# Optimization experiments

Hardware: AMD Instinct MI355X
Metric: run time of the kernel (lower is better)

Reference implementation:

```python
import jax, jax.numpy as jnp
import numpy as np

ERR = 1e-12


def setup_inputs() -> dict:
    key = jax.random.key(0)
    k1, k2, k3 = jax.random.split(key, 3)
    B, H, L, D = 2, 16, 2048, 64
    k = jax.random.normal(k1, (B, H, L, D), dtype=jnp.float32)
    src = jax.random.uniform(k2, (B, H, L), dtype=jnp.float32)
    dest = jax.random.uniform(k3, (B, H, L), dtype=jnp.float32)
    return {"k": k, "src": src, "dest": dest}


def reference(k, src, dest):
    # k: [B,H,L,D], src/dest: [B,H,L]
    L = k.shape[-2]
    s = jnp.sqrt(src + ERR)   # sqrt-scaled source weights
    d = jnp.sqrt(dest + ERR)  # sqrt-scaled destination weights
    # affinity_1[b,h,i,j] = s_i * d_j * (k_i . k_j), fused as (k*s) @ (k*d)^T
    a1 = jnp.einsum("bhid,bhjd->bhij", k * s[..., :, None], k * d[..., :, None])
    # relu then (x+err)^(2/3)  (kernel: exp2(log2(relu(a)+err) * 2/3))
    a3 = jnp.exp2(jnp.log2(jax.nn.relu(a1) + ERR) * (2.0 / 3.0))
    # forward cumulative sum over j, output causally masked to j >= i
    cs = jnp.cumsum(a3, axis=-1)
    idx = jnp.arange(L)
    mask = idx[:, None] <= idx[None, :]  # keep j >= i
    return jnp.where(mask, cs, 0.0)
```

## Files before the change

### kernel.cpp

```cpp
#include <hip/hip_runtime.h>

#define BH   32
#define LSEQ 2048
#define DDIM 64
#define ERRC 1e-12f
#define SROW2 260

typedef __attribute__((ext_vector_type(8)))  short bf16x8;
typedef __attribute__((ext_vector_type(4)))  float floatx4;
typedef __attribute__((ext_vector_type(4)))  unsigned short ushort4v;

__device__ __forceinline__ unsigned short f2bf(float f) {
    unsigned u = __float_as_uint(f);
    u = u + 0x7FFFu + ((u >> 16) & 1u);
    return (unsigned short)(u >> 16);
}

__device__ __forceinline__ bf16x8 pack8s(const float* __restrict__ p, float w) {
    const floatx4* pv = (const floatx4*)p;
    floatx4 x = pv[0], y = pv[1];
    bf16x8 r;
    r[0] = (short)f2bf(x[0] * w); r[1] = (short)f2bf(x[1] * w);
    r[2] = (short)f2bf(x[2] * w); r[3] = (short)f2bf(x[3] * w);
    r[4] = (short)f2bf(y[0] * w); r[5] = (short)f2bf(y[1] * w);
    r[6] = (short)f2bf(y[2] * w); r[7] = (short)f2bf(y[3] * w);
    return r;
}

__global__ __launch_bounds__(256) void prep_kd(const float* __restrict__ k,
                                               const float* __restrict__ dest,
                                               unsigned short* __restrict__ kd) {
    int idx4 = blockIdx.x * 256 + threadIdx.x;
    int row  = idx4 >> 4;
    float d = sqrtf(dest[row] + ERRC);
    floatx4 v = ((const floatx4*)k)[idx4];
    ushort4v od;
#pragma unroll
    for (int r = 0; r < 4; ++r) od[r] = f2bf(v[r] * d);
    ((ushort4v*)kd)[idx4] = od;
}

__device__ __forceinline__ void load_frag(const unsigned short* __restrict__ p,
                                          bf16x8& lo, bf16x8& hi) {
    lo = *(const bf16x8*)p;
    hi = *(const bf16x8*)(p + 32);
}

__device__ __forceinline__ void load_b_raw(const float* __restrict__ k,
                                           const float* __restrict__ src,
                                           int bhL, int row, int q,
                                           bf16x8& lo, bf16x8& hi) {
    const float* p = k + (long)(bhL + row) * DDIM + q * 8;
    float s = sqrtf(src[bhL + row] + ERRC);
    lo = pack8s(p, s);
    hi = pack8s(p + 32, s);
}

__global__ __launch_bounds__(256, 4) void strip_sums(const unsigned short* __restrict__ kd,
                                                     const float* __restrict__ k,
                                                     const float* __restrict__ src,
                                                     float* __restrict__ S) {
    const int tid  = threadIdx.x;
    const int wave = tid >> 6;
    const int lane = tid & 63;
    const int q    = lane >> 4;
    const int l16  = lane & 15;
    const int bh   = blockIdx.x & 31;
    const int ib   = blockIdx.x >> 5;
    const int i0   = (ib * 4 + wave) * 16;
    const int bhL  = bh * LSEQ;
    const unsigned short* kdb = kd + (long)bh * LSEQ * DDIM;

    bf16x8 blo, bhi;
    load_b_raw(k, src, bhL, i0 + l16, q, blo, bhi);

    bf16x8 aLo[4], aHi[4];
#pragma unroll
    for (int t = 0; t < 4; ++t)
        load_frag(kdb + (long)(16 * t + l16) * DDIM + q * 8, aLo[t], aHi[t]);

    const float c23 = 2.0f / 3.0f;
    float ssv[3];

    for (int cc = 0; cc < 3; ++cc) {
        float ss = 0.f;
        for (int g = 0; g < 8; ++g) {
            const int jn = (cc * 8 + g < 23) ? (cc * 512 + g * 64 + 64) : 0;
            bf16x8 nLo[4], nHi[4];
#pragma unroll
            for (int t = 0; t < 4; ++t)
                load_frag(kdb + (long)(jn + 16 * t + l16) * DDIM + q * 8, nLo[t], nHi[t]);

            floatx4 acc[4];
#pragma unroll
            for (int t = 0; t < 4; ++t) {
                floatx4 z4 = {0.f, 0.f, 0.f, 0.f};
                z4 = __builtin_amdgcn_mfma_f32_16x16x32_bf16(aLo[t], blo, z4, 0, 0, 0);
                acc[t] = __builtin_amdgcn_mfma_f32_16x16x32_bf16(aHi[t], bhi, z4, 0, 0, 0);
            }

            float s = 0.f;
#pragma unroll
            for (int t = 0; t < 4; ++t)
#pragma unroll
                for (int r = 0; r < 4; ++r) {
                    float v = fmaxf(acc[t][r], 0.f) + ERRC;
                    s += exp2f(c23 * __log2f(v));
                }
            float s1 = s + __shfl_xor(s, 16, 64);
            ss += s1 + __shfl_xor(s1, 32, 64);

#pragma unroll
            for (int t = 0; t < 4; ++t) { aLo[t] = nLo[t]; aHi[t] = nHi[t]; }
        }
        ssv[cc] = ss;
    }

    float sv = (q == 0) ? ssv[0] : (q == 1) ? ssv[1] : ssv[2];
    if (q < 3)
        S[(long)(bhL + i0 + l16) * 4 + q] = sv;
}

__global__ __launch_bounds__(128, 2) void chunk_out(const unsigned short* __restrict__ kd,
                                                    const float* __restrict__ k,
                                                    const float* __restrict__ src,
                                                    const float* __restrict__ S,
                                                    float* __restrict__ out) {
    __shared__ float strip[2][16 * SROW2];
    const int tid  = threadIdx.x;
    const int wave = tid >> 6;
    const int lane = tid & 63;
    const int q    = lane >> 4;
    const int l16  = lane & 15;
    const int bh   = blockIdx.x & 31;
    const int rr   = blockIdx.x >> 5;
    const int ib2  = rr & 63;
    const int c    = rr >> 6;
    const int i0   = (ib2 * 2 + wave) * 16;
    const int bhL  = bh * LSEQ;
    const int jb   = c << 9;

    if (jb + 512 <= i0) {
        const floatx4 z = {0.f, 0.f, 0.f, 0.f};
#pragma unroll
        for (int s = 0; s < 16; ++s) {
            float* row = out + (long)(bhL + i0 + s) * LSEQ + jb + 4 * lane;
            *(floatx4*)row = z;
            *(floatx4*)(row + 256) = z;
        }
        return;
    }

    const unsigned short* kdb = kd + (long)bh * LSEQ * DDIM;
    float* sw = strip[wave];

    bf16x8 blo, bhi;
    load_b_raw(k, src, bhL, i0 + l16, q, blo, bhi);

    float carry = 0.f;
    const float* Sr = S + (long)(bhL + i0 + l16) * 4;
#pragma unroll
    for (int cc = 0; cc < 3; ++cc)
        if (cc < c) carry += Sr[cc];

    const float c23 = 2.0f / 3.0f;

    bf16x8 aLo[4], aHi[4];
#pragma unroll
    for (int t = 0; t < 4; ++t)
        load_frag(kdb + (long)(jb + 16 * t + l16) * DDIM + q * 8, aLo[t], aHi[t]);

    for (int hh = 0; hh < 2; ++hh) {
#pragma unroll
        for (int gg = 0; gg < 4; ++gg) {
            const int colbase = gg * 64;
            const int j0 = jb + hh * 256 + colbase;
            const int jl = hh * 256 + colbase + 64;
            const int jn = jb + ((jl < 512) ? jl : 0);

            bf16x8 nLo[4], nHi[4];
#pragma unroll
            for (int t = 0; t < 4; ++t)
                load_frag(kdb + (long)(jn + 16 * t + l16) * DDIM + q * 8, nLo[t], nHi[t]);

            floatx4 acc[4];
#pragma unroll
            for (int t = 0; t < 4; ++t) {
                floatx4 z4 = {0.f, 0.f, 0.f, 0.f};
                z4 = __builtin_amdgcn_mfma_f32_16x16x32_bf16(aLo[t], blo, z4, 0, 0, 0);
                acc[t] = __builtin_amdgcn_mfma_f32_16x16x32_bf16(aHi[t], bhi, z4, 0, 0, 0);
            }

            float u[4][4];
#pragma unroll
            for (int t = 0; t < 4; ++t)
#pragma unroll
                for (int r = 0; r < 4; ++r) {
                    float v = fmaxf(acc[t][r], 0.f) + ERRC;
                    u[t][r] = exp2f(c23 * __log2f(v));
                }

            if (j0 + 64 <= i0) {
                float s = 0.f;
#pragma unroll
                for (int t = 0; t < 4; ++t)
                    s += (u[t][0] + u[t][1]) + (u[t][2] + u[t][3]);
                float s1 = s + __shfl_xor(s, 16, 64);
                carry += s1 + __shfl_xor(s1, 32, 64);
                const floatx4 z = {0.f, 0.f, 0.f, 0.f};
#pragma unroll
                for (int t = 0; t < 4; ++t)
                    *(floatx4*)&sw[l16 * SROW2 + colbase + 16 * t + 4 * q] = z;
            } else {
#pragma unroll
                for (int t = 0; t < 4; ++t) {
                    const int jt0 = j0 + 16 * t;
                    float* dst = &sw[l16 * SROW2 + colbase + 16 * t + 4 * q];
                    if (jt0 + 16 <= i0) {
                        float s = (u[t][0] + u[t][1]) + (u[t][2] + u[t][3]);
                        float s1 = s + __shfl_xor(s, 16, 64);
                        carry += s1 + __shfl_xor(s1, 32, 64);
                        const floatx4 z = {0.f, 0.f, 0.f, 0.f};
                        *(floatx4*)dst = z;
                    } else {
                        u[t][1] += u[t][0];
                        u[t][2] += u[t][1];
                        u[t][3] += u[t][2];
                        const float Sg  = u[t][3];
                        const float x16 = __shfl_xor(Sg, 16, 64);
                        const float s1  = Sg + x16;
                        const float x32 = __shfl_xor(s1, 32, 64);
                        const float E = ((q & 1) ? x16 : 0.f) + ((q & 2) ? x32 : 0.f) + carry;
                        carry += s1 + x32;
                        floatx4 o;
                        if (jt0 == i0) {
#pragma unroll
                            for (int r = 0; r < 4; ++r)
                                o[r] = ((q * 4 + r) >= l16) ? (u[t][r] + E) : 0.f;
                        } else {
#pragma unroll
                            for (int r = 0; r < 4; ++r)
                                o[r] = u[t][r] + E;
                        }
                        *(floatx4*)dst = o;
                    }
                }
            }

#pragma unroll
            for (int t = 0; t < 4; ++t) { aLo[t] = nLo[t]; aHi[t] = nHi[t]; }
        }

#pragma unroll
        for (int s = 0; s < 16; ++s) {
            floatx4 v = *(const floatx4*)&sw[s * SROW2 + 4 * lane];
            *(floatx4*)(out + (long)(bhL + i0 + s) * LSEQ + jb + hh * 256 + 4 * lane) = v;
        }
    }
}

__device__ __forceinline__ void load_row16_raw(const float* __restrict__ kp, long base, int row,
                                               int q, const float* __restrict__ w, int bhL,
                                               bf16x8& lo, bf16x8& hi) {
    const float* p = kp + base + (long)row * DDIM + q * 8;
    float s = sqrtf(w[bhL + row] + ERRC);
    lo = pack8s(p, s);
    hi = pack8s(p + 32, s);
}

__global__ __launch_bounds__(256, 4) void mha_raw(const float* __restrict__ kp,
                                                  const float* __restrict__ src,
                                                  const float* __restrict__ dest,
                                                  float* __restrict__ out) {
    const int tid  = threadIdx.x;
    const int wave = tid >> 6;
    const int lane = tid & 63;
    const int q    = lane >> 4;
    const int l16  = lane & 15;
    const int bh = blockIdx.x & 31;
    const int ib = blockIdx.x >> 5;
    const int i0 = (ib * 4 + wave) * 16;
    const int bhL = bh * LSEQ;
    const long base = (long)bh * LSEQ * DDIM;

    bf16x8 blo, bhi;
    load_row16_raw(kp, base, i0 + l16, q, src, bhL, blo, bhi);

    float carry = 0.f;
    const float c23 = 2.0f / 3.0f;

    bf16x8 aLo[4], aHi[4];
#pragma unroll
    for (int t = 0; t < 4; ++t)
        load_row16_raw(kp, base, 16 * t + l16, q, dest, bhL, aLo[t], aHi[t]);

    float* orow = out + (long)(bhL + i0 + l16) * LSEQ + q * 4;

    for (int it = 0; it < 32; ++it) {
        const int j0 = it << 6;
        bf16x8 nLo[4], nHi[4];
        const int jn = (it < 31) ? (j0 + 64) : 0;
#pragma unroll
        for (int t = 0; t < 4; ++t)
            load_row16_raw(kp, base, jn + 16 * t + l16, q, dest, bhL, nLo[t], nHi[t]);

        floatx4 acc[4];
#pragma unroll
        for (int t = 0; t < 4; ++t) {
            floatx4 z4 = {0.f, 0.f, 0.f, 0.f};
            z4 = __builtin_amdgcn_mfma_f32_16x16x32_bf16(aLo[t], blo, z4, 0, 0, 0);
            acc[t] = __builtin_amdgcn_mfma_f32_16x16x32_bf16(aHi[t], bhi, z4, 0, 0, 0);
        }

        float u[4][4];
#pragma unroll
        for (int t = 0; t < 4; ++t)
#pragma unroll
            for (int r = 0; r < 4; ++r) {
                float v = fmaxf(acc[t][r], 0.f) + ERRC;
                u[t][r] = exp2f(c23 * __log2f(v));
            }

#pragma unroll
        for (int t = 0; t < 4; ++t) {
            const int jt0 = j0 + 16 * t;
            if (jt0 + 16 <= i0) {
                float s = (u[t][0] + u[t][1]) + (u[t][2] + u[t][3]);
                float s1 = s + __shfl_xor(s, 16, 64);
                carry += s1 + __shfl_xor(s1, 32, 64);
                const floatx4 z = {0.f, 0.f, 0.f, 0.f};
                *(floatx4*)(orow + jt0) = z;
            } else {
                u[t][1] += u[t][0];
                u[t][2] += u[t][1];
                u[t][3] += u[t][2];
                const float Sg  = u[t][3];
                const float x16 = __shfl_xor(Sg, 16, 64);
                const float s1  = Sg + x16;
                const float x32 = __shfl_xor(s1, 32, 64);
                const float E = ((q & 1) ? x16 : 0.f) + ((q & 2) ? x32 : 0.f) + carry;
                carry += s1 + x32;
                floatx4 o;
                if (jt0 == i0) {
#pragma unroll
                    for (int r = 0; r < 4; ++r)
                        o[r] = ((q * 4 + r) >= l16) ? (u[t][r] + E) : 0.f;
                } else {
#pragma unroll
                    for (int r = 0; r < 4; ++r)
                        o[r] = u[t][r] + E;
                }
                *(floatx4*)(orow + jt0) = o;
            }
        }

#pragma unroll
        for (int t = 0; t < 4; ++t) { aLo[t] = nLo[t]; aHi[t] = nHi[t]; }
    }
}

extern "C" void kernel_launch(void* const* d_in, const int* in_sizes, int n_in,
                              void* d_out, int out_size, void* d_ws, size_t ws_size,
                              hipStream_t stream) {
    const float* k    = (const float*)d_in[0];
    const float* src  = (const float*)d_in[1];
    const float* dest = (const float*)d_in[2];
    float* out = (float*)d_out;

    const size_t kdsz = (size_t)BH * LSEQ * DDIM * sizeof(unsigned short);
    const size_t ssz  = (size_t)BH * LSEQ * 4 * sizeof(float);
    if (ws_size >= kdsz + ssz) {
        unsigned short* kd = (unsigned short*)d_ws;
        float* S = (float*)((char*)d_ws + kdsz);
        prep_kd<<<dim3(4096), dim3(256), 0, stream>>>(k, dest, kd);
        strip_sums<<<dim3(1024), dim3(256), 0, stream>>>(kd, k, src, S);
        chunk_out<<<dim3(8192), dim3(128), 0, stream>>>(kd, k, src, S, out);
    } else {
        mha_raw<<<dim3(1024), dim3(256), 0, stream>>>(k, src, dest, out);
    }
}
```

Measured before the change: 685.7 us.

## Write chunk outputs directly from registers, drop LDS staging, remap block indices

The output kernel no longer stages each 16x256 strip in shared memory and copies it out row-coalesced. Each lane now writes its 16-byte fragments straight to global memory. Removing the LDS lets launch bounds rise to four blocks per SM. Block-to-work mapping is also reordered so adjacent waves cover the four column chunks of the same rows and head, which changes locality and the order work is scheduled. The risk is that the direct writes are less coalesced (each lane writes a different row), which may hurt write efficiency on a write-bound kernel.

```diff
diff --git a/kernel.cpp b/kernel.cpp
--- a/kernel.cpp
+++ b/kernel.cpp
@@ -4,7 +4,6 @@
 #define LSEQ 2048
 #define DDIM 64
 #define ERRC 1e-12f
-#define SROW2 260
 
 typedef __attribute__((ext_vector_type(8)))  short bf16x8;
 typedef __attribute__((ext_vector_type(4)))  float floatx4;
@@ -121,22 +120,21 @@
         S[(long)(bhL + i0 + l16) * 4 + q] = sv;
 }
 
-__global__ __launch_bounds__(128, 2) void chunk_out(const unsigned short* __restrict__ kd,
-                                                    const float* __restrict__ k,
-                                                    const float* __restrict__ src,
-                                                    const float* __restrict__ S,
-                                                    float* __restrict__ out) {
-    __shared__ float strip[2][16 * SROW2];
+__global__ __launch_bounds__(128, 4) void chunk_out2(const unsigned short* __restrict__ kd,
+                                                     const float* __restrict__ k,
+                                                     const float* __restrict__ src,
+                                                     const float* __restrict__ S,
+                                                     float* __restrict__ out) {
     const int tid  = threadIdx.x;
     const int wave = tid >> 6;
     const int lane = tid & 63;
     const int q    = lane >> 4;
     const int l16  = lane & 15;
-    const int bh   = blockIdx.x & 31;
-    const int rr   = blockIdx.x >> 5;
-    const int ib2  = rr & 63;
-    const int c    = rr >> 6;
-    const int i0   = (ib2 * 2 + wave) * 16;
+    const int u    = blockIdx.x * 2 + wave;
+    const int c    = u & 3;
+    const int bh   = (u >> 2) & 31;
+    const int it   = u >> 7;
+    const int i0   = it << 4;
     const int bhL  = bh * LSEQ;
     const int jb   = c << 9;
 
@@ -152,7 +150,6 @@
     }
 
     const unsigned short* kdb = kd + (long)bh * LSEQ * DDIM;
-    float* sw = strip[wave];
 
     bf16x8 blo, bhi;
     load_b_raw(k, src, bhL, i0 + l16, q, blo, bhi);
@@ -170,92 +167,82 @@
     for (int t = 0; t < 4; ++t)
         load_frag(kdb + (long)(jb + 16 * t + l16) * DDIM + q * 8, aLo[t], aHi[t]);
 
-    for (int hh = 0; hh < 2; ++hh) {
-#pragma unroll
-        for (int gg = 0; gg < 4; ++gg) {
-            const int colbase = gg * 64;
-            const int j0 = jb + hh * 256 + colbase;
-            const int jl = hh * 256 + colbase + 64;
-            const int jn = jb + ((jl < 512) ? jl : 0);
-
-            bf16x8 nLo[4], nHi[4];
+    float* orow = out + (long)(bhL + i0 + l16) * LSEQ + q * 4;
+
+    for (int g = 0; g < 8; ++g) {
+        const int j0 = jb + (g << 6);
+        const int jn = jb + ((g < 7) ? ((g + 1) << 6) : 0);
+
+        bf16x8 nLo[4], nHi[4];
+#pragma unroll
+        for (int t = 0; t < 4; ++t)
+            load_frag(kdb + (long)(jn + 16 * t + l16) * DDIM + q * 8, nLo[t], nHi[t]);
+
+        floatx4 acc[4];
+#pragma unroll
+        for (int t = 0; t < 4; ++t) {
+            floatx4 z4 = {0.f, 0.f, 0.f, 0.f};
+            z4 = __builtin_amdgcn_mfma_f32_16x16x32_bf16(aLo[t], blo, z4, 0, 0, 0);
+            acc[t] = __builtin_amdgcn_mfma_f32_16x16x32_bf16(aHi[t], bhi, z4, 0, 0, 0);
+        }
+
+        float uu[4][4];
+#pragma unroll
+        for (int t = 0; t < 4; ++t)
+#pragma unroll
+            for (int r = 0; r < 4; ++r) {
+                float v = fmaxf(acc[t][r], 0.f) + ERRC;
+                uu[t][r] = exp2f(c23 * __log2f(v));
+            }
+
+        if (j0 + 64 <= i0) {
+            float s = 0.f;
 #pragma unroll
             for (int t = 0; t < 4; ++t)
-                load_frag(kdb + (long)(jn + 16 * t + l16) * DDIM + q * 8, nLo[t], nHi[t]);
-
-            floatx4 acc[4];
+                s += (uu[t][0] + uu[t][1]) + (uu[t][2] + uu[t][3]);
+            float s1 = s + __shfl_xor(s, 16, 64);
+            carry += s1 + __shfl_xor(s1, 32, 64);
+            const floatx4 z = {0.f, 0.f, 0.f, 0.f};
+#pragma unroll
+            for (int t = 0; t < 4; ++t)
+                *(floatx4*)(orow + j0 + 16 * t) = z;
+        } else {
 #pragma unroll
             for (int t = 0; t < 4; ++t) {
-                floatx4 z4 = {0.f, 0.f, 0.f, 0.f};
-                z4 = __builtin_amdgcn_mfma_f32_16x16x32_bf16(aLo[t], blo, z4, 0, 0, 0);
-                acc[t] = __builtin_amdgcn_mfma_f32_16x16x32_bf16(aHi[t], bhi, z4, 0, 0, 0);
-            }
-
-            float u[4][4];
-#pragma unroll
-            for (int t = 0; t < 4; ++t)
-#pragma unroll
-                for (int r = 0; r < 4; ++r) {
-                    float v = fmaxf(acc[t][r], 0.f) + ERRC;
-                    u[t][r] = exp2f(c23 * __log2f(v));
+                const int jt0 = j0 + 16 * t;
+                if (jt0 + 16 <= i0) {
+                    float s = (uu[t][0] + uu[t][1]) + (uu[t][2] + uu[t][3]);
+                    float s1 = s + __shfl_xor(s, 16, 64);
+                    carry += s1 + __shfl_xor(s1, 32, 64);
+                    const floatx4 z = {0.f, 0.f, 0.f, 0.f};
+                    *(floatx4*)(orow + jt0) = z;
+                } else {
+                    uu[t][1] += uu[t][0];
+                    uu[t][2] += uu[t][1];
+                    uu[t][3] += uu[t][2];
+                    const float Sg  = uu[t][3];
+                    const float x16 = __shfl_xor(Sg, 16, 64);
+                    const float s1  = Sg + x16;
+                    const float x32 = __shfl_xor(s1, 32, 64);
+                    const float E = ((q & 1) ? x16 : 0.f) + ((q & 2) ? x32 : 0.f) + carry;
+                    carry += s1 + x32;
+                    floatx4 o;
+                    if (jt0 == i0) {
+#pragma unroll
+                        for (int r = 0; r < 4; ++r)
+                            o[r] = ((q * 4 + r) >= l16) ? (uu[t][r] + E) : 0.f;
+                    } else {
+#pragma unroll
+                        for (int r = 0; r < 4; ++r)
+                            o[r] = uu[t][r] + E;
+                    }
+                    *(floatx4*)(orow + jt0) = o;
                 }
-
-            if (j0 + 64 <= i0) {
-                float s = 0.f;
-#pragma unroll
-                for (int t = 0; t < 4; ++t)
-                    s += (u[t][0] + u[t][1]) + (u[t][2] + u[t][3]);
-                float s1 = s + __shfl_xor(s, 16, 64);
-                carry += s1 + __shfl_xor(s1, 32, 64);
-                const floatx4 z = {0.f, 0.f, 0.f, 0.f};
-#pragma unroll
-                for (int t = 0; t < 4; ++t)
-                    *(floatx4*)&sw[l16 * SROW2 + colbase + 16 * t + 4 * q] = z;
-            } else {
-#pragma unroll
-                for (int t = 0; t < 4; ++t) {
-                    const int jt0 = j0 + 16 * t;
-                    float* dst = &sw[l16 * SROW2 + colbase + 16 * t + 4 * q];
-                    if (jt0 + 16 <= i0) {
-                        float s = (u[t][0] + u[t][1]) + (u[t][2] + u[t][3]);
-                        float s1 = s + __shfl_xor(s, 16, 64);
-                        carry += s1 + __shfl_xor(s1, 32, 64);
-                        const floatx4 z = {0.f, 0.f, 0.f, 0.f};
-                        *(floatx4*)dst = z;
-                    } else {
-                        u[t][1] += u[t][0];
-                        u[t][2] += u[t][1];
-                        u[t][3] += u[t][2];
-                        const float Sg  = u[t][3];
-                        const float x16 = __shfl_xor(Sg, 16, 64);
-                        const float s1  = Sg + x16;
-                        const float x32 = __shfl_xor(s1, 32, 64);
-                        const float E = ((q & 1) ? x16 : 0.f) + ((q & 2) ? x32 : 0.f) + carry;
-                        carry += s1 + x32;
-                        floatx4 o;
-                        if (jt0 == i0) {
-#pragma unroll
-                            for (int r = 0; r < 4; ++r)
-                                o[r] = ((q * 4 + r) >= l16) ? (u[t][r] + E) : 0.f;
-                        } else {
-#pragma unroll
-                            for (int r = 0; r < 4; ++r)
-                                o[r] = u[t][r] + E;
-                        }
-                        *(floatx4*)dst = o;
-                    }
-                }
-            }
-
-#pragma unroll
-            for (int t = 0; t < 4; ++t) { aLo[t] = nLo[t]; aHi[t] = nHi[t]; }
-        }
-
-#pragma unroll
-        for (int s = 0; s < 16; ++s) {
-            floatx4 v = *(const floatx4*)&sw[s * SROW2 + 4 * lane];
-            *(floatx4*)(out + (long)(bhL + i0 + s) * LSEQ + jb + hh * 256 + 4 * lane) = v;
-        }
+            }
+        }
+
+#pragma unroll
+        for (int t = 0; t < 4; ++t) { aLo[t] = nLo[t]; aHi[t] = nHi[t]; }
     }
 }
 
@@ -312,29 +299,29 @@
             acc[t] = __builtin_amdgcn_mfma_f32_16x16x32_bf16(aHi[t], bhi, z4, 0, 0, 0);
         }
 
-        float u[4][4];
+        float uu[4][4];
 #pragma unroll
         for (int t = 0; t < 4; ++t)
 #pragma unroll
             for (int r = 0; r < 4; ++r) {
                 float v = fmaxf(acc[t][r], 0.f) + ERRC;
-                u[t][r] = exp2f(c23 * __log2f(v));
+                uu[t][r] = exp2f(c23 * __log2f(v));
             }
 
 #pragma unroll
         for (int t = 0; t < 4; ++t) {
             const int jt0 = j0 + 16 * t;
             if (jt0 + 16 <= i0) {
-                float s = (u[t][0] + u[t][1]) + (u[t][2] + u[t][3]);
+                float s = (uu[t][0] + uu[t][1]) + (uu[t][2] + uu[t][3]);
                 float s1 = s + __shfl_xor(s, 16, 64);
                 carry += s1 + __shfl_xor(s1, 32, 64);
                 const floatx4 z = {0.f, 0.f, 0.f, 0.f};
                 *(floatx4*)(orow + jt0) = z;
             } else {
-                u[t][1] += u[t][0];
-                u[t][2] += u[t][1];
-                u[t][3] += u[t][2];
-                const float Sg  = u[t][3];
+                uu[t][1] += uu[t][0];
+                uu[t][2] += uu[t][1];
+                uu[t][3] += uu[t][2];
+                const float Sg  = uu[t][3];
                 const float x16 = __shfl_xor(Sg, 16, 64);
                 const float s1  = Sg + x16;
                 const float x32 = __shfl_xor(s1, 32, 64);
@@ -344,11 +331,11 @@
                 if (jt0 == i0) {
 #pragma unroll
                     for (int r = 0; r < 4; ++r)
-                        o[r] = ((q * 4 + r) >= l16) ? (u[t][r] + E) : 0.f;
+                        o[r] = ((q * 4 + r) >= l16) ? (uu[t][r] + E) : 0.f;
                 } else {
 #pragma unroll
                     for (int r = 0; r < 4; ++r)
-                        o[r] = u[t][r] + E;
+                        o[r] = uu[t][r] + E;
                 }
                 *(floatx4*)(orow + jt0) = o;
             }
@@ -374,7 +361,7 @@
         float* S = (float*)((char*)d_ws + kdsz);
         prep_kd<<<dim3(4096), dim3(256), 0, stream>>>(k, dest, kd);
         strip_sums<<<dim3(1024), dim3(256), 0, stream>>>(kd, k, src, S);
-        chunk_out<<<dim3(8192), dim3(128), 0, stream>>>(kd, k, src, S, out);
+        chunk_out2<<<dim3(8192), dim3(128), 0, stream>>>(kd, k, src, S, out);
     } else {
         mha_raw<<<dim3(1024), dim3(256), 0, stream>>>(k, src, dest, out);
     }
```

After: 706.9 us. 1.03x slower.
